# Performance work log

Measured on AMD Instinct MI355X. Metric: run time of the kernel, lower is better.

## Reference

```python
import jax, jax.numpy as jnp
import numpy as np

N_NODES = 50000
N_EDGES = 800000
H = 128       # num_hidden
NUM_INV = 32  # num_inv


def _glorot(key, shape):
    fan_in, fan_out = shape[0], shape[1]
    lim = np.sqrt(6.0 / (fan_in + fan_out)).astype(np.float32)
    return jax.random.uniform(key, shape, jnp.float32, -lim, lim)


def setup_inputs() -> dict:
    key = jax.random.key(0)
    ks = jax.random.split(key, 12)
    x = jax.random.normal(ks[0], (N_NODES, H), jnp.float32)
    adj = jax.random.randint(ks[1], (2, N_EDGES), 0, N_NODES, dtype=jnp.int64)
    inv = jax.random.normal(ks[2], (N_EDGES, NUM_INV), jnp.float32)
    # MessageLayer: message_mlp = Linear(2H+inv -> H), SiLU, Linear(H -> H), SiLU
    Wm1 = _glorot(ks[3], (2 * H + NUM_INV, H)); bm1 = jnp.zeros((H,), jnp.float32)
    Wm2 = _glorot(ks[4], (H, H));               bm2 = jnp.zeros((H,), jnp.float32)
    # edge_inf_mlp = Linear(H -> 1), Sigmoid
    We = _glorot(ks[5], (H, 1));                be = jnp.zeros((1,), jnp.float32)
    # UpdateLayer (num_mes=1): update_mlp = Linear(2H -> H), SiLU, Linear(H -> H)
    Wu1 = _glorot(ks[6], (2 * H, H));           bu1 = jnp.zeros((H,), jnp.float32)
    Wu2 = _glorot(ks[7], (H, H));               bu2 = jnp.zeros((H,), jnp.float32)
    return {"x": x, "adj": adj, "inv": inv,
            "Wm1": Wm1, "bm1": bm1, "Wm2": Wm2, "bm2": bm2,
            "We": We, "be": be,
            "Wu1": Wu1, "bu1": bu1, "Wu2": Wu2, "bu2": bu2}


def reference(x, adj, inv, Wm1, bm1, Wm2, bm2, We, be, Wu1, bu1, Wu2, bu2):
    send, rec = adj[0], adj[1]
    # MessageLayer: gather endpoints, concat with invariants, 2-layer SiLU MLP
    state = jnp.concatenate([x[send], x[rec], inv], axis=1)      # [E, 2H+inv]
    h = jax.nn.silu(state @ Wm1 + bm1)                           # [E, H]
    msg = jax.nn.silu(h @ Wm2 + bm2)                             # [E, H]
    gate = jax.nn.sigmoid(msg @ We + be)                         # [E, 1]
    aggr = jax.ops.segment_sum(msg * gate, rec, num_segments=x.shape[0])  # [N, H]
    # UpdateLayer: concat [x, aggregated message], Linear-SiLU-Linear
    upd_in = jnp.concatenate([x, aggr], axis=1)                  # [N, 2H]
    x_up = jax.nn.silu(upd_in @ Wu1 + bu1) @ Wu2 + bu2           # [N, H]
    # Residual add
    return x + x_up
```

## Files before the change

### kernel.cpp

```cpp
#include <hip/hip_runtime.h>
#include <math.h>

#define NNODES 50000
#define NEDGES 800000
#define HDIM 128
#define NINV 32
#define K1 288
#define NTILES_E 25000
#define NTILES_N 1563

#define W1STRIDE 296
#define U1STRIDE 264
#define HSTRIDE 132

typedef float floatx4 __attribute__((ext_vector_type(4)));
typedef short short8  __attribute__((ext_vector_type(8)));

union V4S8 { uint4 u; short8 s; int2 d[2]; };

__device__ __forceinline__ float silu_f(float z) { return z / (1.0f + __expf(-z)); }

__device__ __forceinline__ unsigned short f2bf_rne(float f) {
    unsigned u = __float_as_uint(f);
    u += 0x7fffu + ((u >> 16) & 1u);
    return (unsigned short)(u >> 16);
}

__device__ __forceinline__ unsigned pk_bf(float hi, float lo) {
    return __builtin_amdgcn_perm(__float_as_uint(hi), __float_as_uint(lo), 0x07060302);
}

__device__ __forceinline__ short8 cvt8(float4 f0, float4 f1) {
    V4S8 v;
    v.u.x = pk_bf(f0.y, f0.x);
    v.u.y = pk_bf(f0.w, f0.z);
    v.u.z = pk_bf(f1.y, f1.x);
    v.u.w = pk_bf(f1.w, f1.z);
    return v.s;
}

__device__ __forceinline__ int adj_at(const void* adj, int is64, long long pos) {
    if (is64) return (int)((const long long*)adj)[pos];
    return ((const int*)adj)[pos];
}

__global__ __launch_bounds__(256) void detect_idx64(const int* __restrict__ adj32,
                                                    int* __restrict__ flag) {
    __shared__ int any_nz;
    if (threadIdx.x == 0) any_nz = 0;
    __syncthreads();
    int v = adj32[threadIdx.x * 2 + 1];
    if (v != 0) atomicOr(&any_nz, 1);
    __syncthreads();
    if (threadIdx.x == 0) *flag = (any_nz == 0) ? 1 : 0;
}

__global__ __launch_bounds__(256) void prep_weights(
    const float* __restrict__ Wm1, const float* __restrict__ Wm2,
    const float* __restrict__ Wu1, const float* __restrict__ Wu2,
    unsigned short* __restrict__ Wm1t, unsigned short* __restrict__ Wm2t,
    unsigned short* __restrict__ Wu1t, unsigned short* __restrict__ Wu2t)
{
    int i = blockIdx.x * 256 + threadIdx.x;
    if (i < 128 * K1) {
        int n = i / K1, k = i % K1;
        Wm1t[i] = f2bf_rne(Wm1[k * HDIM + n]);
    } else if ((i -= 128 * K1) < 128 * HDIM) {
        int n = i / HDIM, k = i % HDIM;
        Wm2t[i] = f2bf_rne(Wm2[k * HDIM + n]);
    } else if ((i -= 128 * HDIM) < 128 * 256) {
        int n = i / 256, k = i % 256;
        Wu1t[i] = f2bf_rne(Wu1[k * HDIM + n]);
    } else if ((i -= 128 * 256) < 128 * HDIM) {
        int n = i / HDIM, k = i % HDIM;
        Wu2t[i] = f2bf_rne(Wu2[k * HDIM + n]);
    }
}

__global__ __launch_bounds__(512, 2) void edge_kernel(
    const float* __restrict__ x, const void* __restrict__ adj,
    const int* __restrict__ flagp, const float* __restrict__ inv,
    const unsigned short* __restrict__ Wm1t, const float* __restrict__ bm1,
    const unsigned short* __restrict__ Wm2t, const float* __restrict__ bm2,
    const float* __restrict__ We, const float* __restrict__ be,
    float* __restrict__ aggr)
{
    __shared__ unsigned short s_w1[128 * W1STRIDE];
    __shared__ unsigned short s_h[8 * 32 * HSTRIDE];

    const int t    = threadIdx.x;
    const int is64 = *flagp;
    const int l    = t & 63;
    const int wid  = t >> 6;
    const int l15  = l & 15;
    const int quad = l >> 4;

    for (int idx = t; idx < 128 * 36; idx += 512) {
        int n = idx / 36, c = idx % 36;
        *(uint4*)&s_w1[n * W1STRIDE + c * 8] = *(const uint4*)(Wm1t + n * K1 + c * 8);
    }

    short8 w2f[4][8];
    #pragma unroll
    for (int ks = 0; ks < 4; ++ks)
        #pragma unroll
        for (int nt = 0; nt < 8; ++nt)
            w2f[ks][nt] = *(const short8*)(Wm2t + (nt * 16 + l15) * HDIM + ks * 32 + quad * 8);

    __syncthreads();

    unsigned short* hbuf = s_h + wid * (32 * HSTRIDE);
    const int gwave  = blockIdx.x * 8 + wid;
    const int nwaves = gridDim.x * 8;

    for (int tile = gwave; tile < NTILES_E; tile += nwaves) {
        const int e0 = tile * 32;
        int se[2], re[2];
        unsigned offS[2], offR[2], offI[2];
        #pragma unroll
        for (int m = 0; m < 2; ++m) {
            se[m] = adj_at(adj, is64, e0 + m * 16 + l15);
            re[m] = adj_at(adj, is64, (long long)NEDGES + e0 + m * 16 + l15);
            offS[m] = (unsigned)se[m] * HDIM;
            offR[m] = (unsigned)re[m] * HDIM;
            offI[m] = (unsigned)(e0 + m * 16 + l15) * NINV;
        }

        auto aptr = [&](int s, int m) -> const float* {
            if (s < 4)  return x   + offS[m] + s * 32 + quad * 8;
            if (s < 8)  return x   + offR[m] + (s - 4) * 32 + quad * 8;
            return             inv + offI[m] + quad * 8;
        };

        float4 F0[2][2], F1[2][2];
        #pragma unroll
        for (int m = 0; m < 2; ++m) {
            const float* p = aptr(0, m); F0[m][0] = ((const float4*)p)[0]; F0[m][1] = ((const float4*)p)[1];
            const float* q = aptr(1, m); F1[m][0] = ((const float4*)q)[0]; F1[m][1] = ((const float4*)q)[1];
        }

        floatx4 acc[2][8];
        #pragma unroll
        for (int nt = 0; nt < 8; ++nt) {
            float bv = bm1[nt * 16 + l15];
            acc[0][nt] = (floatx4){bv, bv, bv, bv};
            acc[1][nt] = acc[0][nt];
        }

        #pragma unroll
        for (int s = 0; s < 9; ++s) {
            short8 a[2];
            #pragma unroll
            for (int m = 0; m < 2; ++m) {
                float4 f0 = (s & 1) ? F1[m][0] : F0[m][0];
                float4 f1 = (s & 1) ? F1[m][1] : F0[m][1];
                a[m] = cvt8(f0, f1);
                if (s + 2 <= 8) {
                    const float* p = aptr(s + 2, m);
                    if (s & 1) { F1[m][0] = ((const float4*)p)[0]; F1[m][1] = ((const float4*)p)[1]; }
                    else       { F0[m][0] = ((const float4*)p)[0]; F0[m][1] = ((const float4*)p)[1]; }
                }
            }
            const unsigned short* wbase = s_w1 + l15 * W1STRIDE + s * 32 + quad * 8;
            #pragma unroll
            for (int nt = 0; nt < 8; ++nt) {
                short8 b = *(const short8*)(wbase + nt * 16 * W1STRIDE);
                acc[0][nt] = __builtin_amdgcn_mfma_f32_16x16x32_bf16(a[0], b, acc[0][nt], 0, 0, 0);
                acc[1][nt] = __builtin_amdgcn_mfma_f32_16x16x32_bf16(a[1], b, acc[1][nt], 0, 0, 0);
            }
        }

        #pragma unroll
        for (int m = 0; m < 2; ++m)
            #pragma unroll
            for (int nt = 0; nt < 8; ++nt)
                #pragma unroll
                for (int r = 0; r < 4; ++r) {
                    float hv = silu_f(acc[m][nt][r]);
                    hbuf[(m * 16 + quad * 4 + r) * HSTRIDE + nt * 16 + l15] =
                        (unsigned short)(__float_as_uint(hv) >> 16);
                }

        #pragma unroll
        for (int nt = 0; nt < 8; ++nt) {
            float bv = bm2[nt * 16 + l15];
            acc[0][nt] = (floatx4){bv, bv, bv, bv};
            acc[1][nt] = acc[0][nt];
        }

        #pragma unroll
        for (int ks = 0; ks < 4; ++ks) {
            short8 a2[2];
            #pragma unroll
            for (int m = 0; m < 2; ++m) {
                int base = (m * 16 + l15) * HSTRIDE + ks * 32 + quad * 8;
                V4S8 v;
                v.d[0] = *(const int2*)(hbuf + base);
                v.d[1] = *(const int2*)(hbuf + base + 4);
                a2[m] = v.s;
            }
            #pragma unroll
            for (int nt = 0; nt < 8; ++nt) {
                acc[0][nt] = __builtin_amdgcn_mfma_f32_16x16x32_bf16(a2[0], w2f[ks][nt], acc[0][nt], 0, 0, 0);
                acc[1][nt] = __builtin_amdgcn_mfma_f32_16x16x32_bf16(a2[1], w2f[ks][nt], acc[1][nt], 0, 0, 0);
            }
        }

        float be0 = be[0];
        #pragma unroll
        for (int m = 0; m < 2; ++m) {
            #pragma unroll
            for (int nt = 0; nt < 8; ++nt)
                #pragma unroll
                for (int r = 0; r < 4; ++r)
                    acc[m][nt][r] = silu_f(acc[m][nt][r]);

            #pragma unroll
            for (int r = 0; r < 4; ++r) {
                float part = 0.f;
                #pragma unroll
                for (int nt = 0; nt < 8; ++nt)
                    part = fmaf(acc[m][nt][r], We[nt * 16 + l15], part);
                part += __shfl_xor(part, 1);
                part += __shfl_xor(part, 2);
                part += __shfl_xor(part, 4);
                part += __shfl_xor(part, 8);
                float g = 1.0f / (1.0f + __expf(-(part + be0)));
                int rr = __shfl(re[m], quad * 4 + r, 16);
                float* dst = aggr + (long long)rr * HDIM + l15;
                #pragma unroll
                for (int nt = 0; nt < 8; ++nt)
                    atomicAdd(dst + nt * 16, acc[m][nt][r] * g);
            }
        }
    }
}

__global__ __launch_bounds__(256) void node_kernel(
    const float* __restrict__ x, const float* __restrict__ aggr,
    const unsigned short* __restrict__ Wu1t, const float* __restrict__ bu1,
    const unsigned short* __restrict__ Wu2t, const float* __restrict__ bu2,
    float* __restrict__ out)
{
    __shared__ unsigned short s_u1[128 * U1STRIDE];
    __shared__ unsigned short s_h[4 * 32 * HSTRIDE];

    const int t    = threadIdx.x;
    const int l    = t & 63;
    const int wid  = t >> 6;
    const int l15  = l & 15;
    const int quad = l >> 4;

    for (int idx = t; idx < 128 * 32; idx += 256) {
        int n = idx / 32, c = idx % 32;
        *(uint4*)&s_u1[n * U1STRIDE + c * 8] = *(const uint4*)(Wu1t + n * 256 + c * 8);
    }

    short8 w2f[4][8];
    #pragma unroll
    for (int ks = 0; ks < 4; ++ks)
        #pragma unroll
        for (int nt = 0; nt < 8; ++nt)
            w2f[ks][nt] = *(const short8*)(Wu2t + (nt * 16 + l15) * HDIM + ks * 32 + quad * 8);

    __syncthreads();

    unsigned short* hbuf = s_h + wid * (32 * HSTRIDE);
    const int tile = blockIdx.x * 4 + wid;
    if (tile >= NTILES_N) return;
    const int n0 = tile * 32;

    unsigned offX[2];
    #pragma unroll
    for (int m = 0; m < 2; ++m) {
        int row = n0 + m * 16 + l15;
        if (row >= NNODES) row = NNODES - 1;
        offX[m] = (unsigned)row * HDIM;
    }

    floatx4 acc[2][8];
    #pragma unroll
    for (int nt = 0; nt < 8; ++nt) {
        float bv = bu1[nt * 16 + l15];
        acc[0][nt] = (floatx4){bv, bv, bv, bv};
        acc[1][nt] = acc[0][nt];
    }

    #pragma unroll
    for (int s = 0; s < 8; ++s) {
        short8 a[2];
        #pragma unroll
        for (int m = 0; m < 2; ++m) {
            const float* p = (s < 4) ? (x + offX[m] + s * 32 + quad * 8)
                                     : (aggr + offX[m] + (s - 4) * 32 + quad * 8);
            float4 f0 = ((const float4*)p)[0];
            float4 f1 = ((const float4*)p)[1];
            a[m] = cvt8(f0, f1);
        }
        const unsigned short* wbase = s_u1 + l15 * U1STRIDE + s * 32 + quad * 8;
        #pragma unroll
        for (int nt = 0; nt < 8; ++nt) {
            short8 b = *(const short8*)(wbase + nt * 16 * U1STRIDE);
            acc[0][nt] = __builtin_amdgcn_mfma_f32_16x16x32_bf16(a[0], b, acc[0][nt], 0, 0, 0);
            acc[1][nt] = __builtin_amdgcn_mfma_f32_16x16x32_bf16(a[1], b, acc[1][nt], 0, 0, 0);
        }
    }

    #pragma unroll
    for (int m = 0; m < 2; ++m)
        #pragma unroll
        for (int nt = 0; nt < 8; ++nt)
            #pragma unroll
            for (int r = 0; r < 4; ++r) {
                float hv = silu_f(acc[m][nt][r]);
                hbuf[(m * 16 + quad * 4 + r) * HSTRIDE + nt * 16 + l15] =
                    (unsigned short)(__float_as_uint(hv) >> 16);
            }

    #pragma unroll
    for (int nt = 0; nt < 8; ++nt) {
        float bv = bu2[nt * 16 + l15];
        acc[0][nt] = (floatx4){bv, bv, bv, bv};
        acc[1][nt] = acc[0][nt];
    }

    #pragma unroll
    for (int ks = 0; ks < 4; ++ks) {
        short8 a2[2];
        #pragma unroll
        for (int m = 0; m < 2; ++m) {
            int base = (m * 16 + l15) * HSTRIDE + ks * 32 + quad * 8;
            V4S8 v;
            v.d[0] = *(const int2*)(hbuf + base);
            v.d[1] = *(const int2*)(hbuf + base + 4);
            a2[m] = v.s;
        }
        #pragma unroll
        for (int nt = 0; nt < 8; ++nt) {
            acc[0][nt] = __builtin_amdgcn_mfma_f32_16x16x32_bf16(a2[0], w2f[ks][nt], acc[0][nt], 0, 0, 0);
            acc[1][nt] = __builtin_amdgcn_mfma_f32_16x16x32_bf16(a2[1], w2f[ks][nt], acc[1][nt], 0, 0, 0);
        }
    }

    #pragma unroll
    for (int m = 0; m < 2; ++m)
        #pragma unroll
        for (int r = 0; r < 4; ++r) {
            int row = n0 + m * 16 + quad * 4 + r;
            if (row < NNODES) {
                #pragma unroll
                for (int nt = 0; nt < 8; ++nt) {
                    int col = nt * 16 + l15;
                    out[(long long)row * HDIM + col] = x[(long long)row * HDIM + col] + acc[m][nt][r];
                }
            }
        }
}

extern "C" void kernel_launch(void* const* d_in, const int* in_sizes, int n_in,
                              void* d_out, int out_size, void* d_ws, size_t ws_size,
                              hipStream_t stream)
{
    const float* x   = (const float*)d_in[0];
    const void*  adj = d_in[1];
    const float* inv = (const float*)d_in[2];
    const float* Wm1 = (const float*)d_in[3];
    const float* bm1 = (const float*)d_in[4];
    const float* Wm2 = (const float*)d_in[5];
    const float* bm2 = (const float*)d_in[6];
    const float* We  = (const float*)d_in[7];
    const float* be  = (const float*)d_in[8];
    const float* Wu1 = (const float*)d_in[9];
    const float* bu1 = (const float*)d_in[10];
    const float* Wu2 = (const float*)d_in[11];
    const float* bu2 = (const float*)d_in[12];
    float* out = (float*)d_out;

    char* ws = (char*)d_ws;
    float* aggr = (float*)ws;
    size_t off = (size_t)NNODES * HDIM * 4;
    int* flag = (int*)(ws + off);            off += 16;
    unsigned short* Wm1t = (unsigned short*)(ws + off);  off += 128 * K1 * 2;
    unsigned short* Wm2t = (unsigned short*)(ws + off);  off += 128 * HDIM * 2;
    unsigned short* Wu1t = (unsigned short*)(ws + off);  off += 128 * 256 * 2;
    unsigned short* Wu2t = (unsigned short*)(ws + off);

    hipMemsetAsync(aggr, 0, (size_t)NNODES * HDIM * sizeof(float), stream);
    detect_idx64<<<1, 256, 0, stream>>>((const int*)adj, flag);
    prep_weights<<<400, 256, 0, stream>>>(Wm1, Wm2, Wu1, Wu2, Wm1t, Wm2t, Wu1t, Wu2t);
    edge_kernel<<<256, 512, 0, stream>>>(x, adj, flag, inv,
                                         Wm1t, bm1, Wm2t, bm2, We, be, aggr);
    node_kernel<<<(NTILES_N + 3) / 4, 256, 0, stream>>>(x, aggr,
                                                        Wu1t, bu1, Wu2t, bu2, out);
}
```

Measured before the change: 675.1 us.

## Pre-convert x to bf16, move W2 to LDS, 16-edge tiles with cross-tile prefetch

Adds a pass that converts x (and later aggr) to bf16 in workspace, so the edge kernel gathers half the bytes per endpoint and skips per-tile conversion. The edge kernel switches to 1024-thread blocks with 16-edge wave tiles, stores Wm2 in LDS instead of registers, hoists biases into registers, and prefetches the next tile's gathered rows while running the current MFMAs. The hidden activations pass through a small double-buffered LDS chunk interleaved with the second GEMM. The node kernel is restructured the same way. The cost is two extra conversion kernels and extra workspace traffic, and the switch from truncation to round-to-nearest when writing hidden activations to bf16 adds ALU work.

```diff
diff --git a/kernel.cpp b/kernel.cpp
--- a/kernel.cpp
+++ b/kernel.cpp
@@ -6,36 +6,33 @@
 #define HDIM 128
 #define NINV 32
 #define K1 288
-#define NTILES_E 25000
-#define NTILES_N 1563
-
-#define W1STRIDE 296
-#define U1STRIDE 264
-#define HSTRIDE 132
+#define NTILE_E 50000
+#define NTILE_N 3125
+
+#define W1S 296
+#define W2S 136
+#define U1S 264
+#define HCS 40
 
 typedef float floatx4 __attribute__((ext_vector_type(4)));
 typedef short short8  __attribute__((ext_vector_type(8)));
-
-union V4S8 { uint4 u; short8 s; int2 d[2]; };
+union U4S8 { uint4 u; short8 s; };
 
 __device__ __forceinline__ float silu_f(float z) { return z / (1.0f + __expf(-z)); }
-
-__device__ __forceinline__ unsigned short f2bf_rne(float f) {
+__device__ __forceinline__ unsigned rnd_bf(float f) {
     unsigned u = __float_as_uint(f);
-    u += 0x7fffu + ((u >> 16) & 1u);
-    return (unsigned short)(u >> 16);
-}
-
-__device__ __forceinline__ unsigned pk_bf(float hi, float lo) {
-    return __builtin_amdgcn_perm(__float_as_uint(hi), __float_as_uint(lo), 0x07060302);
-}
-
-__device__ __forceinline__ short8 cvt8(float4 f0, float4 f1) {
-    V4S8 v;
-    v.u.x = pk_bf(f0.y, f0.x);
-    v.u.y = pk_bf(f0.w, f0.z);
-    v.u.z = pk_bf(f1.y, f1.x);
-    v.u.w = pk_bf(f1.w, f1.z);
+    return u + 0x7fffu + ((u >> 16) & 1u);
+}
+__device__ __forceinline__ unsigned short bf_rne(float f) { return (unsigned short)(rnd_bf(f) >> 16); }
+__device__ __forceinline__ unsigned pk2(unsigned rlo, unsigned rhi) {
+    return __builtin_amdgcn_perm(rhi, rlo, 0x07060302);
+}
+__device__ __forceinline__ short8 cvt8_rne(float4 a, float4 b) {
+    U4S8 v;
+    v.u.x = pk2(rnd_bf(a.x), rnd_bf(a.y));
+    v.u.y = pk2(rnd_bf(a.z), rnd_bf(a.w));
+    v.u.z = pk2(rnd_bf(b.x), rnd_bf(b.y));
+    v.u.w = pk2(rnd_bf(b.z), rnd_bf(b.w));
     return v.s;
 }
 
@@ -64,29 +61,50 @@
     int i = blockIdx.x * 256 + threadIdx.x;
     if (i < 128 * K1) {
         int n = i / K1, k = i % K1;
-        Wm1t[i] = f2bf_rne(Wm1[k * HDIM + n]);
+        Wm1t[i] = bf_rne(Wm1[k * HDIM + n]);
     } else if ((i -= 128 * K1) < 128 * HDIM) {
         int n = i / HDIM, k = i % HDIM;
-        Wm2t[i] = f2bf_rne(Wm2[k * HDIM + n]);
+        Wm2t[i] = bf_rne(Wm2[k * HDIM + n]);
     } else if ((i -= 128 * HDIM) < 128 * 256) {
         int n = i / 256, k = i % 256;
-        Wu1t[i] = f2bf_rne(Wu1[k * HDIM + n]);
+        Wu1t[i] = bf_rne(Wu1[k * HDIM + n]);
     } else if ((i -= 128 * 256) < 128 * HDIM) {
         int n = i / HDIM, k = i % HDIM;
-        Wu2t[i] = f2bf_rne(Wu2[k * HDIM + n]);
-    }
-}
-
-__global__ __launch_bounds__(512, 2) void edge_kernel(
-    const float* __restrict__ x, const void* __restrict__ adj,
+        Wu2t[i] = bf_rne(Wu2[k * HDIM + n]);
+    }
+}
+
+__global__ __launch_bounds__(256) void cvt_f32_bf16(const float* __restrict__ src,
+                                                    unsigned short* __restrict__ dst) {
+    int i = blockIdx.x * 256 + threadIdx.x;
+    float4 v = ((const float4*)src)[i];
+    ushort4 o;
+    o.x = bf_rne(v.x); o.y = bf_rne(v.y); o.z = bf_rne(v.z); o.w = bf_rne(v.w);
+    ((ushort4*)dst)[i] = o;
+}
+
+#define MF8W1(aa) { _Pragma("unroll") for (int nt = 0; nt < 8; ++nt) { \
+    short8 bb = *(const short8*)(wb1 + nt * 16 * W1S); \
+    acc[nt] = __builtin_amdgcn_mfma_f32_16x16x32_bf16(aa, bb, acc[nt], 0, 0, 0); } }
+
+#define LDW(off, col) (*(const uint4*)(xb + (off) + (col) * 32 + quad * 8))
+
+#define WRCH(k) { unsigned short* hb = hc + (((k) & 1) ? 640 : 0); \
+    _Pragma("unroll") for (int j = 0; j < 2; ++j) \
+    _Pragma("unroll") for (int r = 0; r < 4; ++r) \
+        hb[(quad * 4 + r) * HCS + j * 16 + l15] = bf_rne(silu_f(acc[2 * (k) + j][r])); }
+
+__global__ __launch_bounds__(1024, 4) void edge_kernel(
+    const unsigned short* __restrict__ xb, const void* __restrict__ adj,
     const int* __restrict__ flagp, const float* __restrict__ inv,
     const unsigned short* __restrict__ Wm1t, const float* __restrict__ bm1,
     const unsigned short* __restrict__ Wm2t, const float* __restrict__ bm2,
     const float* __restrict__ We, const float* __restrict__ be,
     float* __restrict__ aggr)
 {
-    __shared__ unsigned short s_w1[128 * W1STRIDE];
-    __shared__ unsigned short s_h[8 * 32 * HSTRIDE];
+    __shared__ unsigned short s_w1[128 * W1S];
+    __shared__ unsigned short s_w2[128 * W2S];
+    __shared__ unsigned short s_hc[16 * 1280];
 
     const int t    = threadIdx.x;
     const int is64 = *flagp;
@@ -95,155 +113,130 @@
     const int l15  = l & 15;
     const int quad = l >> 4;
 
-    for (int idx = t; idx < 128 * 36; idx += 512) {
+    for (int idx = t; idx < 128 * 36; idx += 1024) {
         int n = idx / 36, c = idx % 36;
-        *(uint4*)&s_w1[n * W1STRIDE + c * 8] = *(const uint4*)(Wm1t + n * K1 + c * 8);
-    }
-
-    short8 w2f[4][8];
-    #pragma unroll
-    for (int ks = 0; ks < 4; ++ks)
+        *(uint4*)&s_w1[n * W1S + c * 8] = *(const uint4*)(Wm1t + n * K1 + c * 8);
+    }
+    for (int idx = t; idx < 128 * 16; idx += 1024) {
+        int n = idx / 16, c = idx % 16;
+        *(uint4*)&s_w2[n * W2S + c * 8] = *(const uint4*)(Wm2t + n * HDIM + c * 8);
+    }
+
+    float bm1v[8], bm2v[8], Wev[8];
+    #pragma unroll
+    for (int nt = 0; nt < 8; ++nt) {
+        bm1v[nt] = bm1[nt * 16 + l15];
+        bm2v[nt] = bm2[nt * 16 + l15];
+        Wev[nt]  = We[nt * 16 + l15];
+    }
+    const float be0 = be[0];
+
+    __syncthreads();
+
+    unsigned short* hc = s_hc + wid * 1280;
+    const int nwav = gridDim.x * 16;
+    int tile = blockIdx.x * 16 + wid;
+
+    int se = adj_at(adj, is64, (long long)tile * 16 + l15);
+    int re = adj_at(adj, is64, (long long)NEDGES + tile * 16 + l15);
+    unsigned oS = (unsigned)se * HDIM, oR = (unsigned)re * HDIM;
+    uint4 P0 = LDW(oS, 0), P1 = LDW(oS, 1), P2 = LDW(oS, 2);
+    float4 Pi0, Pi1;
+    {
+        const float* ip = inv + (long long)(tile * 16 + l15) * NINV + quad * 8;
+        Pi0 = ((const float4*)ip)[0]; Pi1 = ((const float4*)ip)[1];
+    }
+
+    for (; tile < NTILE_E; tile += nwav) {
+        const int next = tile + nwav;
+        const int ne0  = (next < NTILE_E ? next : 0) * 16;
+        int nse = adj_at(adj, is64, ne0 + l15);
+        int nre = adj_at(adj, is64, (long long)NEDGES + ne0 + l15);
+        unsigned noS, noR;
+
+        floatx4 acc[8];
         #pragma unroll
         for (int nt = 0; nt < 8; ++nt)
-            w2f[ks][nt] = *(const short8*)(Wm2t + (nt * 16 + l15) * HDIM + ks * 32 + quad * 8);
-
-    __syncthreads();
-
-    unsigned short* hbuf = s_h + wid * (32 * HSTRIDE);
-    const int gwave  = blockIdx.x * 8 + wid;
-    const int nwaves = gridDim.x * 8;
-
-    for (int tile = gwave; tile < NTILES_E; tile += nwaves) {
-        const int e0 = tile * 32;
-        int se[2], re[2];
-        unsigned offS[2], offR[2], offI[2];
-        #pragma unroll
-        for (int m = 0; m < 2; ++m) {
-            se[m] = adj_at(adj, is64, e0 + m * 16 + l15);
-            re[m] = adj_at(adj, is64, (long long)NEDGES + e0 + m * 16 + l15);
-            offS[m] = (unsigned)se[m] * HDIM;
-            offR[m] = (unsigned)re[m] * HDIM;
-            offI[m] = (unsigned)(e0 + m * 16 + l15) * NINV;
-        }
-
-        auto aptr = [&](int s, int m) -> const float* {
-            if (s < 4)  return x   + offS[m] + s * 32 + quad * 8;
-            if (s < 8)  return x   + offR[m] + (s - 4) * 32 + quad * 8;
-            return             inv + offI[m] + quad * 8;
-        };
-
-        float4 F0[2][2], F1[2][2];
-        #pragma unroll
-        for (int m = 0; m < 2; ++m) {
-            const float* p = aptr(0, m); F0[m][0] = ((const float4*)p)[0]; F0[m][1] = ((const float4*)p)[1];
-            const float* q = aptr(1, m); F1[m][0] = ((const float4*)q)[0]; F1[m][1] = ((const float4*)q)[1];
-        }
-
-        floatx4 acc[2][8];
-        #pragma unroll
-        for (int nt = 0; nt < 8; ++nt) {
-            float bv = bm1[nt * 16 + l15];
-            acc[0][nt] = (floatx4){bv, bv, bv, bv};
-            acc[1][nt] = acc[0][nt];
-        }
-
-        #pragma unroll
-        for (int s = 0; s < 9; ++s) {
-            short8 a[2];
-            #pragma unroll
-            for (int m = 0; m < 2; ++m) {
-                float4 f0 = (s & 1) ? F1[m][0] : F0[m][0];
-                float4 f1 = (s & 1) ? F1[m][1] : F0[m][1];
-                a[m] = cvt8(f0, f1);
-                if (s + 2 <= 8) {
-                    const float* p = aptr(s + 2, m);
-                    if (s & 1) { F1[m][0] = ((const float4*)p)[0]; F1[m][1] = ((const float4*)p)[1]; }
-                    else       { F0[m][0] = ((const float4*)p)[0]; F0[m][1] = ((const float4*)p)[1]; }
-                }
+            acc[nt] = (floatx4){bm1v[nt], bm1v[nt], bm1v[nt], bm1v[nt]};
+
+        {
+            U4S8 c; short8 a;
+            const unsigned short* wb1;
+            c.u = P0; a = c.s; P0 = LDW(oS, 3); wb1 = s_w1 + l15 * W1S + 0 * 32 + quad * 8; MF8W1(a);
+            c.u = P1; a = c.s; P1 = LDW(oR, 0); wb1 = s_w1 + l15 * W1S + 1 * 32 + quad * 8; MF8W1(a);
+            c.u = P2; a = c.s; P2 = LDW(oR, 1); wb1 = s_w1 + l15 * W1S + 2 * 32 + quad * 8; MF8W1(a);
+            c.u = P0; a = c.s; P0 = LDW(oR, 2); wb1 = s_w1 + l15 * W1S + 3 * 32 + quad * 8; MF8W1(a);
+            c.u = P1; a = c.s; P1 = LDW(oR, 3); wb1 = s_w1 + l15 * W1S + 4 * 32 + quad * 8; MF8W1(a);
+            noS = (unsigned)nse * HDIM; noR = (unsigned)nre * HDIM;
+            c.u = P2; a = c.s; P2 = LDW(noS, 0); wb1 = s_w1 + l15 * W1S + 5 * 32 + quad * 8; MF8W1(a);
+            c.u = P0; a = c.s; P0 = LDW(noS, 1); wb1 = s_w1 + l15 * W1S + 6 * 32 + quad * 8; MF8W1(a);
+            c.u = P1; a = c.s; P1 = LDW(noS, 2); wb1 = s_w1 + l15 * W1S + 7 * 32 + quad * 8; MF8W1(a);
+            a = cvt8_rne(Pi0, Pi1);
+            {
+                const float* ip = inv + (long long)(ne0 + l15) * NINV + quad * 8;
+                Pi0 = ((const float4*)ip)[0]; Pi1 = ((const float4*)ip)[1];
             }
-            const unsigned short* wbase = s_w1 + l15 * W1STRIDE + s * 32 + quad * 8;
+            wb1 = s_w1 + l15 * W1S + 8 * 32 + quad * 8; MF8W1(a);
+        }
+
+        floatx4 acc2[8];
+        #pragma unroll
+        for (int nt = 0; nt < 8; ++nt)
+            acc2[nt] = (floatx4){bm2v[nt], bm2v[nt], bm2v[nt], bm2v[nt]};
+
+        WRCH(0);
+        #pragma unroll
+        for (int ks = 0; ks < 4; ++ks) {
+            if (ks == 0) WRCH(1);
+            if (ks == 1) WRCH(2);
+            if (ks == 2) WRCH(3);
+            U4S8 av; av.u = *(const uint4*)(hc + ((ks & 1) ? 640 : 0) + l15 * HCS + quad * 8);
+            short8 a2 = av.s;
             #pragma unroll
             for (int nt = 0; nt < 8; ++nt) {
-                short8 b = *(const short8*)(wbase + nt * 16 * W1STRIDE);
-                acc[0][nt] = __builtin_amdgcn_mfma_f32_16x16x32_bf16(a[0], b, acc[0][nt], 0, 0, 0);
-                acc[1][nt] = __builtin_amdgcn_mfma_f32_16x16x32_bf16(a[1], b, acc[1][nt], 0, 0, 0);
+                short8 bb = *(const short8*)(s_w2 + (nt * 16 + l15) * W2S + ks * 32 + quad * 8);
+                acc2[nt] = __builtin_amdgcn_mfma_f32_16x16x32_bf16(a2, bb, acc2[nt], 0, 0, 0);
             }
         }
 
         #pragma unroll
-        for (int m = 0; m < 2; ++m)
+        for (int nt = 0; nt < 8; ++nt)
+            #pragma unroll
+            for (int r = 0; r < 4; ++r)
+                acc2[nt][r] = silu_f(acc2[nt][r]);
+
+        #pragma unroll
+        for (int r = 0; r < 4; ++r) {
+            float part = 0.f;
+            #pragma unroll
+            for (int nt = 0; nt < 8; ++nt) part = fmaf(acc2[nt][r], Wev[nt], part);
+            part += __shfl_xor(part, 1);
+            part += __shfl_xor(part, 2);
+            part += __shfl_xor(part, 4);
+            part += __shfl_xor(part, 8);
+            float g = 1.0f / (1.0f + __expf(-(part + be0)));
+            int rr = __shfl(re, quad * 4 + r, 16);
+            float* dst = aggr + (long long)rr * HDIM + l15;
             #pragma unroll
             for (int nt = 0; nt < 8; ++nt)
-                #pragma unroll
-                for (int r = 0; r < 4; ++r) {
-                    float hv = silu_f(acc[m][nt][r]);
-                    hbuf[(m * 16 + quad * 4 + r) * HSTRIDE + nt * 16 + l15] =
-                        (unsigned short)(__float_as_uint(hv) >> 16);
-                }
-
-        #pragma unroll
-        for (int nt = 0; nt < 8; ++nt) {
-            float bv = bm2[nt * 16 + l15];
-            acc[0][nt] = (floatx4){bv, bv, bv, bv};
-            acc[1][nt] = acc[0][nt];
-        }
-
-        #pragma unroll
-        for (int ks = 0; ks < 4; ++ks) {
-            short8 a2[2];
-            #pragma unroll
-            for (int m = 0; m < 2; ++m) {
-                int base = (m * 16 + l15) * HSTRIDE + ks * 32 + quad * 8;
-                V4S8 v;
-                v.d[0] = *(const int2*)(hbuf + base);
-                v.d[1] = *(const int2*)(hbuf + base + 4);
-                a2[m] = v.s;
-            }
-            #pragma unroll
-            for (int nt = 0; nt < 8; ++nt) {
-                acc[0][nt] = __builtin_amdgcn_mfma_f32_16x16x32_bf16(a2[0], w2f[ks][nt], acc[0][nt], 0, 0, 0);
-                acc[1][nt] = __builtin_amdgcn_mfma_f32_16x16x32_bf16(a2[1], w2f[ks][nt], acc[1][nt], 0, 0, 0);
-            }
-        }
-
-        float be0 = be[0];
-        #pragma unroll
-        for (int m = 0; m < 2; ++m) {
-            #pragma unroll
-            for (int nt = 0; nt < 8; ++nt)
-                #pragma unroll
-                for (int r = 0; r < 4; ++r)
-                    acc[m][nt][r] = silu_f(acc[m][nt][r]);
-
-            #pragma unroll
-            for (int r = 0; r < 4; ++r) {
-                float part = 0.f;
-                #pragma unroll
-                for (int nt = 0; nt < 8; ++nt)
-                    part = fmaf(acc[m][nt][r], We[nt * 16 + l15], part);
-                part += __shfl_xor(part, 1);
-                part += __shfl_xor(part, 2);
-                part += __shfl_xor(part, 4);
-                part += __shfl_xor(part, 8);
-                float g = 1.0f / (1.0f + __expf(-(part + be0)));
-                int rr = __shfl(re[m], quad * 4 + r, 16);
-                float* dst = aggr + (long long)rr * HDIM + l15;
-                #pragma unroll
-                for (int nt = 0; nt < 8; ++nt)
-                    atomicAdd(dst + nt * 16, acc[m][nt][r] * g);
-            }
-        }
-    }
-}
-
-__global__ __launch_bounds__(256) void node_kernel(
-    const float* __restrict__ x, const float* __restrict__ aggr,
+                atomicAdd(dst + nt * 16, acc2[nt][r] * g);
+        }
+
+        uint4 tmp = P2; P2 = P1; P1 = P0; P0 = tmp;
+        oS = noS; oR = noR; re = nre;
+    }
+}
+
+__global__ __launch_bounds__(512) void node_kernel(
+    const float* __restrict__ x, const unsigned short* __restrict__ xb,
+    const unsigned short* __restrict__ aggrb,
     const unsigned short* __restrict__ Wu1t, const float* __restrict__ bu1,
     const unsigned short* __restrict__ Wu2t, const float* __restrict__ bu2,
     float* __restrict__ out)
 {
-    __shared__ unsigned short s_u1[128 * U1STRIDE];
-    __shared__ unsigned short s_h[4 * 32 * HSTRIDE];
+    __shared__ unsigned short s_u1[128 * U1S];
+    __shared__ unsigned short s_w2[128 * W2S];
+    __shared__ unsigned short s_hc[8 * 1280];
 
     const int t    = threadIdx.x;
     const int l    = t & 63;
@@ -251,110 +244,81 @@
     const int l15  = l & 15;
     const int quad = l >> 4;
 
-    for (int idx = t; idx < 128 * 32; idx += 256) {
+    for (int idx = t; idx < 128 * 32; idx += 512) {
         int n = idx / 32, c = idx % 32;
-        *(uint4*)&s_u1[n * U1STRIDE + c * 8] = *(const uint4*)(Wu1t + n * 256 + c * 8);
-    }
-
-    short8 w2f[4][8];
-    #pragma unroll
-    for (int ks = 0; ks < 4; ++ks)
+        *(uint4*)&s_u1[n * U1S + c * 8] = *(const uint4*)(Wu1t + n * 256 + c * 8);
+    }
+    for (int idx = t; idx < 128 * 16; idx += 512) {
+        int n = idx / 16, c = idx % 16;
+        *(uint4*)&s_w2[n * W2S + c * 8] = *(const uint4*)(Wu2t + n * HDIM + c * 8);
+    }
+
+    float bu1v[8], bu2v[8];
+    #pragma unroll
+    for (int nt = 0; nt < 8; ++nt) {
+        bu1v[nt] = bu1[nt * 16 + l15];
+        bu2v[nt] = bu2[nt * 16 + l15];
+    }
+
+    __syncthreads();
+
+    const int tile = blockIdx.x * 8 + wid;
+    if (tile >= NTILE_N) return;
+    const int n0 = tile * 16;
+    const unsigned oX = (unsigned)(n0 + l15) * HDIM;
+
+    uint4 A[8];
+    #pragma unroll
+    for (int s = 0; s < 4; ++s) A[s]     = *(const uint4*)(xb    + oX + s * 32 + quad * 8);
+    #pragma unroll
+    for (int s = 0; s < 4; ++s) A[s + 4] = *(const uint4*)(aggrb + oX + s * 32 + quad * 8);
+
+    floatx4 acc[8];
+    #pragma unroll
+    for (int nt = 0; nt < 8; ++nt)
+        acc[nt] = (floatx4){bu1v[nt], bu1v[nt], bu1v[nt], bu1v[nt]};
+
+    #pragma unroll
+    for (int s = 0; s < 8; ++s) {
+        U4S8 c; c.u = A[s]; short8 a = c.s;
+        const unsigned short* wb = s_u1 + l15 * U1S + s * 32 + quad * 8;
+        #pragma unroll
+        for (int nt = 0; nt < 8; ++nt) {
+            short8 bb = *(const short8*)(wb + nt * 16 * U1S);
+            acc[nt] = __builtin_amdgcn_mfma_f32_16x16x32_bf16(a, bb, acc[nt], 0, 0, 0);
+        }
+    }
+
+    floatx4 acc2[8];
+    #pragma unroll
+    for (int nt = 0; nt < 8; ++nt)
+        acc2[nt] = (floatx4){bu2v[nt], bu2v[nt], bu2v[nt], bu2v[nt]};
+
+    unsigned short* hc = s_hc + wid * 1280;
+    WRCH(0);
+    #pragma unroll
+    for (int ks = 0; ks < 4; ++ks) {
+        if (ks == 0) WRCH(1);
+        if (ks == 1) WRCH(2);
+        if (ks == 2) WRCH(3);
+        U4S8 av; av.u = *(const uint4*)(hc + ((ks & 1) ? 640 : 0) + l15 * HCS + quad * 8);
+        short8 a2 = av.s;
+        #pragma unroll
+        for (int nt = 0; nt < 8; ++nt) {
+            short8 bb = *(const short8*)(s_w2 + (nt * 16 + l15) * W2S + ks * 32 + quad * 8);
+            acc2[nt] = __builtin_amdgcn_mfma_f32_16x16x32_bf16(a2, bb, acc2[nt], 0, 0, 0);
+        }
+    }
+
+    #pragma unroll
+    for (int r = 0; r < 4; ++r) {
+        int row = n0 + quad * 4 + r;
+        const float* xr = x + (long long)row * HDIM + l15;
+        float* orow = out + (long long)row * HDIM + l15;
         #pragma unroll
         for (int nt = 0; nt < 8; ++nt)
-            w2f[ks][nt] = *(const short8*)(Wu2t + (nt * 16 + l15) * HDIM + ks * 32 + quad * 8);
-
-    __syncthreads();
-
-    unsigned short* hbuf = s_h + wid * (32 * HSTRIDE);
-    const int tile = blockIdx.x * 4 + wid;
-    if (tile >= NTILES_N) return;
-    const int n0 = tile * 32;
-
-    unsigned offX[2];
-    #pragma unroll
-    for (int m = 0; m < 2; ++m) {
-        int row = n0 + m * 16 + l15;
-        if (row >= NNODES) row = NNODES - 1;
-        offX[m] = (unsigned)row * HDIM;
-    }
-
-    floatx4 acc[2][8];
-    #pragma unroll
-    for (int nt = 0; nt < 8; ++nt) {
-        float bv = bu1[nt * 16 + l15];
-        acc[0][nt] = (floatx4){bv, bv, bv, bv};
-        acc[1][nt] = acc[0][nt];
-    }
-
-    #pragma unroll
-    for (int s = 0; s < 8; ++s) {
-        short8 a[2];
-        #pragma unroll
-        for (int m = 0; m < 2; ++m) {
-            const float* p = (s < 4) ? (x + offX[m] + s * 32 + quad * 8)
-                                     : (aggr + offX[m] + (s - 4) * 32 + quad * 8);
-            float4 f0 = ((const float4*)p)[0];
-            float4 f1 = ((const float4*)p)[1];
-            a[m] = cvt8(f0, f1);
-        }
-        const unsigned short* wbase = s_u1 + l15 * U1STRIDE + s * 32 + quad * 8;
-        #pragma unroll
-        for (int nt = 0; nt < 8; ++nt) {
-            short8 b = *(const short8*)(wbase + nt * 16 * U1STRIDE);
-            acc[0][nt] = __builtin_amdgcn_mfma_f32_16x16x32_bf16(a[0], b, acc[0][nt], 0, 0, 0);
-            acc[1][nt] = __builtin_amdgcn_mfma_f32_16x16x32_bf16(a[1], b, acc[1][nt], 0, 0, 0);
-        }
-    }
-
-    #pragma unroll
-    for (int m = 0; m < 2; ++m)
-        #pragma unroll
-        for (int nt = 0; nt < 8; ++nt)
-            #pragma unroll
-            for (int r = 0; r < 4; ++r) {
-                float hv = silu_f(acc[m][nt][r]);
-                hbuf[(m * 16 + quad * 4 + r) * HSTRIDE + nt * 16 + l15] =
-                    (unsigned short)(__float_as_uint(hv) >> 16);
-            }
-
-    #pragma unroll
-    for (int nt = 0; nt < 8; ++nt) {
-        float bv = bu2[nt * 16 + l15];
-        acc[0][nt] = (floatx4){bv, bv, bv, bv};
-        acc[1][nt] = acc[0][nt];
-    }
-
-    #pragma unroll
-    for (int ks = 0; ks < 4; ++ks) {
-        short8 a2[2];
-        #pragma unroll
-        for (int m = 0; m < 2; ++m) {
-            int base = (m * 16 + l15) * HSTRIDE + ks * 32 + quad * 8;
-            V4S8 v;
-            v.d[0] = *(const int2*)(hbuf + base);
-            v.d[1] = *(const int2*)(hbuf + base + 4);
-            a2[m] = v.s;
-        }
-        #pragma unroll
-        for (int nt = 0; nt < 8; ++nt) {
-            acc[0][nt] = __builtin_amdgcn_mfma_f32_16x16x32_bf16(a2[0], w2f[ks][nt], acc[0][nt], 0, 0, 0);
-            acc[1][nt] = __builtin_amdgcn_mfma_f32_16x16x32_bf16(a2[1], w2f[ks][nt], acc[1][nt], 0, 0, 0);
-        }
-    }
-
-    #pragma unroll
-    for (int m = 0; m < 2; ++m)
-        #pragma unroll
-        for (int r = 0; r < 4; ++r) {
-            int row = n0 + m * 16 + quad * 4 + r;
-            if (row < NNODES) {
-                #pragma unroll
-                for (int nt = 0; nt < 8; ++nt) {
-                    int col = nt * 16 + l15;
-                    out[(long long)row * HDIM + col] = x[(long long)row * HDIM + col] + acc[m][nt][r];
-                }
-            }
-        }
+            orow[nt * 16] = xr[nt * 16] + acc2[nt][r];
+    }
 }
 
 extern "C" void kernel_launch(void* const* d_in, const int* in_sizes, int n_in,
@@ -377,19 +341,23 @@
     float* out = (float*)d_out;
 
     char* ws = (char*)d_ws;
-    float* aggr = (float*)ws;
-    size_t off = (size_t)NNODES * HDIM * 4;
-    int* flag = (int*)(ws + off);            off += 16;
-    unsigned short* Wm1t = (unsigned short*)(ws + off);  off += 128 * K1 * 2;
-    unsigned short* Wm2t = (unsigned short*)(ws + off);  off += 128 * HDIM * 2;
-    unsigned short* Wu1t = (unsigned short*)(ws + off);  off += 128 * 256 * 2;
-    unsigned short* Wu2t = (unsigned short*)(ws + off);
+    size_t off = 0;
+    float* aggr = (float*)(ws + off);                 off += (size_t)NNODES * HDIM * 4;
+    int* flag = (int*)(ws + off);                     off += 16;
+    unsigned short* Wm1t = (unsigned short*)(ws + off); off += 128 * K1 * 2;
+    unsigned short* Wm2t = (unsigned short*)(ws + off); off += 128 * HDIM * 2;
+    unsigned short* Wu1t = (unsigned short*)(ws + off); off += 128 * 256 * 2;
+    unsigned short* Wu2t = (unsigned short*)(ws + off); off += 128 * HDIM * 2;
+    unsigned short* xb    = (unsigned short*)(ws + off); off += (size_t)NNODES * HDIM * 2;
+    unsigned short* aggrb = (unsigned short*)(ws + off);
 
     hipMemsetAsync(aggr, 0, (size_t)NNODES * HDIM * sizeof(float), stream);
     detect_idx64<<<1, 256, 0, stream>>>((const int*)adj, flag);
     prep_weights<<<400, 256, 0, stream>>>(Wm1, Wm2, Wu1, Wu2, Wm1t, Wm2t, Wu1t, Wu2t);
-    edge_kernel<<<256, 512, 0, stream>>>(x, adj, flag, inv,
-                                         Wm1t, bm1, Wm2t, bm2, We, be, aggr);
-    node_kernel<<<(NTILES_N + 3) / 4, 256, 0, stream>>>(x, aggr,
-                                                        Wu1t, bu1, Wu2t, bu2, out);
-}
+    cvt_f32_bf16<<<NNODES * HDIM / 4 / 256, 256, 0, stream>>>(x, xb);
+    edge_kernel<<<256, 1024, 0, stream>>>(xb, adj, flag, inv,
+                                          Wm1t, bm1, Wm2t, bm2, We, be, aggr);
+    cvt_f32_bf16<<<NNODES * HDIM / 4 / 256, 256, 0, stream>>>(aggr, aggrb);
+    node_kernel<<<(NTILE_N + 7) / 8, 512, 0, stream>>>(x, xb, aggrb,
+                                                       Wu1t, bu1, Wu2t, bu2, out);
+}
```

New measurement: 1.802 ms. +167.0%, slower.
